# Kernel tuning notes

Hardware: AMD Instinct MI355X
Metric: run time of the kernel (lower is better)

The kernel has to match this reference:

```python
import jax, jax.numpy as jnp
import numpy as np

B, M, D, K = 512, 32, 2048, 3
COUPLING_STRENGTH = 0.1
SPATIAL_DECAY = 2.0


def setup_inputs() -> dict:
    key = jax.random.key(0)
    k1, k2 = jax.random.split(key)
    x = jax.random.normal(k1, (B, M, D), dtype=jnp.float32)  # stacked module activities
    w = jax.random.normal(k2, (D, K), dtype=jnp.float32) * 0.1  # conv1d weight [out=D, in=1, K] squeezed
    return {"x": x, "w": w}


def reference(x, w):
    # x: [B, M, D] stacked module activities; w: [D, K] field-propagation conv weight.
    b, m, d = x.shape
    k = w.shape[1]
    pad = k // 2
    # Conv1d(in=1, out=D, padding=pad) followed by mean over the length dim is
    # exactly: E[b,m,c] = (1/D) * sum_k w[c,k] * S_k, where S_k is the sum of x
    # over the input positions actually touched by tap k (zero padding drops edges).
    T = x.sum(-1)                       # [B, M] total sum
    cs = jnp.cumsum(x, axis=-1)         # [B, M, D] prefix sums
    S_list = []
    for kk in range(k):                 # K is a small static constant
        o = kk - pad                    # tap offset; touched indices [max(0,o), D-1+min(0,o)]
        if o > 0:
            S_list.append(T - cs[..., o - 1])       # drop first o entries
        elif o < 0:
            S_list.append(cs[..., d - 1 + o])       # drop last |o| entries
        else:
            S_list.append(T)
    S = jnp.stack(S_list, axis=-1)      # [B, M, K]
    fields = jnp.einsum('bmk,dk->bmd', S, w) / d  # electric fields [B, M, D]
    # distance-decayed coupling with self-term excluded (i != j in the loop)
    idx = jnp.arange(m)
    decay = jnp.exp(-jnp.abs(idx[:, None] - idx[None, :]).astype(x.dtype) / SPATIAL_DECAY)
    decay = decay * (1.0 - jnp.eye(m, dtype=x.dtype))  # zero diagonal
    weighted = jnp.einsum('ij,bjd->bid', decay, fields)  # [B, M, D]
    return x + COUPLING_STRENGTH * weighted
```

## Files before the change

kernel.cpp:

```cpp
#include <hip/hip_runtime.h>

#define B_ 512
#define M_ 32
#define D_ 2048

__global__ __launch_bounds__(1024, 4) void ephaptic_fused(const float* __restrict__ x,
                                                          const float* __restrict__ w,
                                                          float* __restrict__ out) {
    const int b = blockIdx.x;
    const int tid = threadIdx.x;
    const int m = tid >> 5;
    const int t = tid & 31;

    __shared__ float sT[M_], sF[M_], sL[M_];
    __shared__ float4 sC[M_ + 1];

    const size_t rowbase = ((size_t)b * M_ + m) * (size_t)D_;
    const float4* row = (const float4*)(x + rowbase);

    float4 v[16];
    float sum = 0.f;
#pragma unroll
    for (int q = 0; q < 16; ++q) {
        v[q] = row[t + 32 * q];
        sum += (v[q].x + v[q].y) + (v[q].z + v[q].w);
    }
#pragma unroll
    for (int q = 0; q < 16; ++q)
        asm volatile("" : "+v"(v[q].x), "+v"(v[q].y), "+v"(v[q].z), "+v"(v[q].w));

#pragma unroll
    for (int off = 16; off > 0; off >>= 1)
        sum += __shfl_xor(sum, off, 64);
    if (t == 0)  { sT[m] = sum; sF[m] = v[0].x; }
    if (t == 31) { sL[m] = v[15].w; }
    __syncthreads();

    if (tid < M_) {
        const int i = tid;
        float r0 = 0.f, r1 = 0.f, r2 = 0.f;
        for (int j = 0; j < M_; ++j) {
            if (j == i) continue;
            const float dij = __expf(-0.5f * fabsf((float)(i - j)));
            const float T = sT[j];
            r0 += dij * (T - sL[j]);
            r1 += dij * T;
            r2 += dij * (T - sF[j]);
        }
        const float s = 0.1f / (float)D_;
        sC[i] = make_float4(r0 * s, r1 * s, r2 * s, 0.f);
    }
    __syncthreads();

    const float4 co = sC[m];
    const float4* wf = (const float4*)w;
    float4* orow = (float4*)(out + rowbase);
#pragma unroll
    for (int q = 0; q < 16; ++q) {
        const int c4 = t + 32 * q;
        const float4 w0 = wf[c4 * 3 + 0];
        const float4 w1 = wf[c4 * 3 + 1];
        const float4 w2 = wf[c4 * 3 + 2];
        float4 o;
        o.x = v[q].x + co.x * w0.x + co.y * w0.y + co.z * w0.z;
        o.y = v[q].y + co.x * w0.w + co.y * w1.x + co.z * w1.y;
        o.z = v[q].z + co.x * w1.z + co.y * w1.w + co.z * w2.x;
        o.w = v[q].w + co.x * w2.y + co.y * w2.z + co.z * w2.w;
        orow[c4] = o;
    }
}

extern "C" void kernel_launch(void* const* d_in, const int* in_sizes, int n_in,
                              void* d_out, int out_size, void* d_ws, size_t ws_size,
                              hipStream_t stream) {
    const float* x = (const float*)d_in[0];
    const float* w = (const float*)d_in[1];
    float* out = (float*)d_out;
    ephaptic_fused<<<B_, 1024, 0, stream>>>(x, w, out);
}
```

Baseline: 55.34 us.

## Remap threads to column-major slices so w loads once per thread, add nontemporal stores

Each thread now owns one float4 column position across 16 rows instead of 16 positions of one row. The w weights are loaded once per thread and reused for all rows, rather than reloaded for every float4. Row sums are computed with per-row wave reductions plus a shared-memory partial table, and the 32x32 coupling is spread across wave lanes with shuffles instead of running serially on 32 threads. Output uses nontemporal stores. The cost is more shuffles and 16 accumulators held in registers per thread.

```diff
diff --git a/kernel.cpp b/kernel.cpp
--- a/kernel.cpp
+++ b/kernel.cpp
@@ -4,69 +4,95 @@
 #define M_ 32
 #define D_ 2048
 
+typedef float fvec4 __attribute__((ext_vector_type(4)));
+
 __global__ __launch_bounds__(1024, 4) void ephaptic_fused(const float* __restrict__ x,
                                                           const float* __restrict__ w,
                                                           float* __restrict__ out) {
     const int b = blockIdx.x;
     const int tid = threadIdx.x;
-    const int m = tid >> 5;
-    const int t = tid & 31;
+    const int wv = tid >> 6;
+    const int lane = tid & 63;
+    const int h = wv >> 3;
+    const int p = tid & 511;
 
-    __shared__ float sT[M_], sF[M_], sL[M_];
-    __shared__ float4 sC[M_ + 1];
+    __shared__ float sF[M_], sL[M_];
+    __shared__ float swv[16][16];
 
-    const size_t rowbase = ((size_t)b * M_ + m) * (size_t)D_;
-    const float4* row = (const float4*)(x + rowbase);
+    const float* xb = x + (size_t)b * M_ * D_;
+    float* ob = out + (size_t)b * M_ * D_;
 
-    float4 v[16];
-    float sum = 0.f;
+    const fvec4* wf = (const fvec4*)w;
+    const fvec4 w0 = wf[p * 3 + 0];
+    const fvec4 w1 = wf[p * 3 + 1];
+    const fvec4 w2 = wf[p * 3 + 2];
+
+    fvec4 v[16];
+    float s[16];
 #pragma unroll
-    for (int q = 0; q < 16; ++q) {
-        v[q] = row[t + 32 * q];
-        sum += (v[q].x + v[q].y) + (v[q].z + v[q].w);
+    for (int r = 0; r < 16; ++r) {
+        v[r] = ((const fvec4*)(xb + (size_t)(h * 16 + r) * D_))[p];
+        s[r] = (v[r].x + v[r].y) + (v[r].z + v[r].w);
     }
 #pragma unroll
-    for (int q = 0; q < 16; ++q)
-        asm volatile("" : "+v"(v[q].x), "+v"(v[q].y), "+v"(v[q].z), "+v"(v[q].w));
-
+    for (int off = 32; off > 0; off >>= 1) {
 #pragma unroll
-    for (int off = 16; off > 0; off >>= 1)
-        sum += __shfl_xor(sum, off, 64);
-    if (t == 0)  { sT[m] = sum; sF[m] = v[0].x; }
-    if (t == 31) { sL[m] = v[15].w; }
-    __syncthreads();
-
-    if (tid < M_) {
-        const int i = tid;
-        float r0 = 0.f, r1 = 0.f, r2 = 0.f;
-        for (int j = 0; j < M_; ++j) {
-            if (j == i) continue;
-            const float dij = __expf(-0.5f * fabsf((float)(i - j)));
-            const float T = sT[j];
-            r0 += dij * (T - sL[j]);
-            r1 += dij * T;
-            r2 += dij * (T - sF[j]);
-        }
-        const float s = 0.1f / (float)D_;
-        sC[i] = make_float4(r0 * s, r1 * s, r2 * s, 0.f);
+        for (int r = 0; r < 16; ++r) s[r] += __shfl_xor(s[r], off, 64);
+    }
+    if (lane == 0) {
+#pragma unroll
+        for (int r = 0; r < 16; ++r) swv[wv][r] = s[r];
+    }
+    if (p == 0) {
+#pragma unroll
+        for (int r = 0; r < 16; ++r) sF[h * 16 + r] = v[r].x;
+    }
+    if (p == 511) {
+#pragma unroll
+        for (int r = 0; r < 16; ++r) sL[h * 16 + r] = v[r].w;
     }
     __syncthreads();
 
-    const float4 co = sC[m];
-    const float4* wf = (const float4*)w;
-    float4* orow = (float4*)(out + rowbase);
+    float a0, a1, a2;
+    {
+        const int j = lane & 31;
+        const int jh = j >> 4;
+        float T = 0.f;
 #pragma unroll
-    for (int q = 0; q < 16; ++q) {
-        const int c4 = t + 32 * q;
-        const float4 w0 = wf[c4 * 3 + 0];
-        const float4 w1 = wf[c4 * 3 + 1];
-        const float4 w2 = wf[c4 * 3 + 2];
-        float4 o;
-        o.x = v[q].x + co.x * w0.x + co.y * w0.y + co.z * w0.z;
-        o.y = v[q].y + co.x * w0.w + co.y * w1.x + co.z * w1.y;
-        o.z = v[q].z + co.x * w1.z + co.y * w1.w + co.z * w2.x;
-        o.w = v[q].w + co.x * w2.y + co.y * w2.z + co.z * w2.w;
-        orow[c4] = o;
+        for (int k = 0; k < 8; ++k) T += swv[jh * 8 + k][j & 15];
+        a1 = T;
+        a0 = T - sL[j];
+        a2 = T - sF[j];
+    }
+    const int ri = lane >> 2;
+    const int q = lane & 3;
+    const int i = h * 16 + ri;
+    float r0 = 0.f, r1 = 0.f, r2 = 0.f;
+#pragma unroll
+    for (int it = 0; it < 8; ++it) {
+        const int j = q + 4 * it;
+        const float d = (j == i) ? 0.f : __expf(-0.5f * fabsf((float)(i - j)));
+        r0 += d * __shfl(a0, j, 64);
+        r1 += d * __shfl(a1, j, 64);
+        r2 += d * __shfl(a2, j, 64);
+    }
+    r0 += __shfl_xor(r0, 1, 64); r0 += __shfl_xor(r0, 2, 64);
+    r1 += __shfl_xor(r1, 1, 64); r1 += __shfl_xor(r1, 2, 64);
+    r2 += __shfl_xor(r2, 1, 64); r2 += __shfl_xor(r2, 2, 64);
+    const float sc = 0.1f / (float)D_;
+    r0 *= sc; r1 *= sc; r2 *= sc;
+
+#pragma unroll
+    for (int r = 0; r < 16; ++r) {
+        const float c0 = __shfl(r0, 4 * r, 64);
+        const float c1 = __shfl(r1, 4 * r, 64);
+        const float c2 = __shfl(r2, 4 * r, 64);
+        fvec4 o;
+        o.x = v[r].x + c0 * w0.x + c1 * w0.y + c2 * w0.z;
+        o.y = v[r].y + c0 * w0.w + c1 * w1.x + c2 * w1.y;
+        o.z = v[r].z + c0 * w1.z + c1 * w1.w + c2 * w2.x;
+        o.w = v[r].w + c0 * w2.y + c1 * w2.z + c2 * w2.w;
+        __builtin_nontemporal_store(o, ((fvec4*)(ob + (size_t)(h * 16 + r) * D_)) + p);
     }
 }
 
```

Measured after the change: 69.42 us. 25.4% more time.
